# Performance work log

Hardware: AMD Instinct MI355X
Metric: run time of the kernel (lower is better)

Reference implementation:

```python
import jax, jax.numpy as jnp
import numpy as np

EPS = 1e-5
SHARE = 8  # share_planes

def batchnorm(x, gamma, beta):
    # BatchNorm1d over the point (batch) dimension, training-mode stats
    mu = jnp.mean(x, axis=0, keepdims=True)
    var = jnp.var(x, axis=0, keepdims=True)
    return gamma * (x - mu) * jax.lax.rsqrt(var + EPS) + beta

def setup_inputs() -> dict:
    key = jax.random.key(0)
    ks = jax.random.split(key, 12)
    N, K, C = 100000, 16, 64
    s = 0.05
    return {
        "p": jax.random.normal(ks[0], (N, 3), jnp.float32),
        "x": jax.random.normal(ks[1], (N, C), jnp.float32),
        "knn_idx": jax.random.randint(ks[2], (N, K), 0, N, jnp.int32),
        "W1": jax.random.normal(ks[3], (C, C), jnp.float32) * s,
        "Wv": jax.random.normal(ks[4], (C, C), jnp.float32) * s,
        "Wp1": jax.random.normal(ks[5], (3, C), jnp.float32) * s,
        "Wp2": jax.random.normal(ks[6], (C, C), jnp.float32) * s,
        "Ww": jax.random.normal(ks[7], (C, C // SHARE), jnp.float32) * s,
        "W3": jax.random.normal(ks[8], (C, C), jnp.float32) * s,
        "g1": jnp.ones((C,), jnp.float32), "b1": jnp.zeros((C,), jnp.float32),
        "g2": jnp.ones((C,), jnp.float32), "b2": jnp.zeros((C,), jnp.float32),
        "g3": jnp.ones((C,), jnp.float32), "b3": jnp.zeros((C,), jnp.float32),
    }

def reference(p, x, knn_idx, W1, Wv, Wp1, Wp2, Ww, W3, g1, b1, g2, b2, g3, b3):
    # PointMixerBlock: linear1/bn1 -> intra-set mixing/bn2 -> linear3/bn3 + residual
    identity = x
    h = jax.nn.relu(batchnorm(x @ W1, g1, b1))              # [N, C]
    # --- PointMixer intra-set layer (gather-compute-aggregate) ---
    v = h @ Wv                                               # values [N, C]
    pj = p[knn_idx]                                          # [N, K, 3] neighbor coords
    delta = pj - p[:, None, :]                               # relative positions
    e = jax.nn.relu(delta @ Wp1) @ Wp2                       # pos encoding [N, K, C]
    hj = h[knn_idx]                                          # neighbor feats [N, K, C]
    energy = (hj + e) @ Ww                                   # [N, K, C//SHARE]
    w = jax.nn.softmax(energy, axis=1)                       # mix over K neighbors
    w = jnp.repeat(w, SHARE, axis=2)                         # share weights across channel groups
    mixed = jnp.sum(w * (v[knn_idx] + e), axis=1)            # [N, C]
    # -------------------------------------------------------------
    h = jax.nn.relu(batchnorm(mixed, g2, b2))
    h = batchnorm(h @ W3, g3, b3)
    return jax.nn.relu(h + identity)
```

## Files before the change

kernel.cpp:

```cpp
#include <hip/hip_runtime.h>
#include <hip/hip_fp16.h>

#define EPSV 1e-5f
#define PST 2048
#define GRID_GEMM 782
#define GRID_MIX  1024
#define GRID_ELT  1024

typedef _Float16 h2_t  __attribute__((ext_vector_type(2)));
typedef __fp16   fp16x2 __attribute__((ext_vector_type(2)));
typedef _Float16 f16x4 __attribute__((ext_vector_type(4)));
typedef _Float16 f16x8 __attribute__((ext_vector_type(8)));
typedef float    f32x4 __attribute__((ext_vector_type(4)));
typedef unsigned short u16;

__device__ __forceinline__ float frelu(float x) { return fmaxf(x, 0.f); }

__device__ __forceinline__ unsigned int pkrtz(float lo, float hi) {
  fp16x2 h = __builtin_amdgcn_cvt_pkrtz(lo, hi);
  return __builtin_bit_cast(unsigned int, h);
}
__device__ __forceinline__ u16 f16b(float x) {
  return (u16)(pkrtz(x, 0.f) & 0xffffu);
}
__device__ __forceinline__ float f16tof(u16 u) {
  return (float)(*reinterpret_cast<const _Float16*>(&u));
}
__device__ __forceinline__ f16x8 mk8(unsigned a, unsigned b, unsigned c, unsigned d) {
  uint4 u; u.x = a; u.y = b; u.z = c; u.w = d;
  return __builtin_bit_cast(f16x8, u);
}
__device__ __forceinline__ f16x4 mk4(unsigned a, unsigned b) {
  uint2 u; u.x = a; u.y = b;
  return __builtin_bit_cast(f16x4, u);
}
__device__ __forceinline__ f32x4 mfma16(f16x8 a, f16x8 b, f32x4 c) {
  return __builtin_amdgcn_mfma_f32_16x16x32_f16(a, b, c, 0, 0, 0);
}
__device__ __forceinline__ f32x4 mfma16k16(f16x4 a, f16x4 b, f32x4 c) {
  return __builtin_amdgcn_mfma_f32_16x16x16f16(a, b, c, 0, 0, 0);
}
__device__ __forceinline__ unsigned relu2(unsigned u) {
  const unsigned m = ((u & 0x80008000u) >> 15) * 0xFFFFu;
  return u & ~m;
}

__global__ __launch_bounds__(256) void pack_k(
    const float* __restrict__ Wp2, const float* __restrict__ Ww,
    const float* __restrict__ Wp1,
    uint4* __restrict__ wwf, uint4* __restrict__ wp2f, uint4* __restrict__ w1f)
{
  __shared__ float wwl[512];
  const int t = threadIdx.x, a = t >> 2, qq = t & 3;
  float acc[8] = {0,0,0,0,0,0,0,0};
#pragma unroll
  for (int cc = 0; cc < 16; ++cc) {
    const int c = qq*16 + cc;
    const float wv = Wp2[a*64 + c];
#pragma unroll
    for (int g = 0; g < 8; ++g) acc[g] = fmaf(wv, Ww[c*8 + g], acc[g]);
  }
#pragma unroll
  for (int g = 0; g < 8; ++g) {
    acc[g] += __shfl_xor(acc[g], 1);
    acc[g] += __shfl_xor(acc[g], 2);
  }
  if (qq == 0) {
#pragma unroll
    for (int g = 0; g < 8; ++g) wwl[a*8 + g] = acc[g];
  }
  __syncthreads();
  if (t < 128) {
    const int h = t >> 6, l = t & 63, r16 = l & 15, q = l >> 4;
    uint4 u = {0,0,0,0};
    if (r16 < 8) {
      unsigned c0 = pkrtz(wwl[(32*h+8*q+0)*8 + r16], wwl[(32*h+8*q+1)*8 + r16]);
      unsigned c1 = pkrtz(wwl[(32*h+8*q+2)*8 + r16], wwl[(32*h+8*q+3)*8 + r16]);
      unsigned c2 = pkrtz(wwl[(32*h+8*q+4)*8 + r16], wwl[(32*h+8*q+5)*8 + r16]);
      unsigned c3 = pkrtz(wwl[(32*h+8*q+6)*8 + r16], wwl[(32*h+8*q+7)*8 + r16]);
      u.x = c0; u.y = c1; u.z = c2; u.w = c3;
    }
    wwf[t] = u;
  }
  for (int e = t; e < 512; e += 256) {
    const int tt = e >> 7, h = (e >> 6) & 1, l = e & 63;
    const int c = 16*tt + (l & 15), q = l >> 4;
    const int d0 = 32*h + 8*q;
    uint4 u;
    u.x = pkrtz(Wp2[(d0+0)*64 + c], Wp2[(d0+1)*64 + c]);
    u.y = pkrtz(Wp2[(d0+2)*64 + c], Wp2[(d0+3)*64 + c]);
    u.z = pkrtz(Wp2[(d0+4)*64 + c], Wp2[(d0+5)*64 + c]);
    u.w = pkrtz(Wp2[(d0+6)*64 + c], Wp2[(d0+7)*64 + c]);
    wp2f[e] = u;
  }
  for (int e = t; e < 384; e += 256) {
    const int r = e >> 7, h = (e >> 6) & 1, l = e & 63, q = l >> 4;
    const int d0 = 32*h + 8*q;
    uint4 u;
    u.x = pkrtz(Wp1[r*64 + d0+0], Wp1[r*64 + d0+1]);
    u.y = pkrtz(Wp1[r*64 + d0+2], Wp1[r*64 + d0+3]);
    u.z = pkrtz(Wp1[r*64 + d0+4], Wp1[r*64 + d0+5]);
    u.w = pkrtz(Wp1[r*64 + d0+6], Wp1[r*64 + d0+7]);
    w1f[e] = u;
  }
}

template<int MODE, bool INF16>
__global__ __launch_bounds__(256, 4) void gemm_mfma_k(
    const void* __restrict__ in, const float* __restrict__ W,
    const float* __restrict__ Ww, const float* __restrict__ ss,
    u16* __restrict__ out16, u16* __restrict__ outw16,
    float* __restrict__ partials, int N)
{
  __shared__ float red[512];
  __shared__ u16 xh[4][16*72];
  const int t = threadIdx.x, lane = t & 63, w = t >> 6;
  const int r16 = lane & 15, q = lane >> 4;
  u16* const xw = &xh[w][0];

  f16x8 bw[2][4];
#pragma unroll
  for (int kb = 0; kb < 2; ++kb) {
#pragma unroll
    for (int tt = 0; tt < 4; ++tt) {
      const int kbase = 32*kb + 8*q;
      const int cc = 16*tt + r16;
      unsigned u0 = pkrtz(W[(kbase+0)*64 + cc], W[(kbase+1)*64 + cc]);
      unsigned u1 = pkrtz(W[(kbase+2)*64 + cc], W[(kbase+3)*64 + cc]);
      unsigned u2 = pkrtz(W[(kbase+4)*64 + cc], W[(kbase+5)*64 + cc]);
      unsigned u3 = pkrtz(W[(kbase+6)*64 + cc], W[(kbase+7)*64 + cc]);
      bw[kb][tt] = mk8(u0, u1, u2, u3);
    }
  }
  f16x8 bg[2];
  if (MODE == 1) {
#pragma unroll
    for (int kb = 0; kb < 2; ++kb) {
      const int kbase = 32*kb + 8*q;
      unsigned u[4];
#pragma unroll
      for (int mm = 0; mm < 4; ++mm) {
        float g0 = (r16 < 8) ? Ww[(kbase + 2*mm    )*8 + r16] : 0.f;
        float g1 = (r16 < 8) ? Ww[(kbase + 2*mm + 1)*8 + r16] : 0.f;
        u[mm] = pkrtz(g0, g1);
      }
      bg[kb] = mk8(u[0], u[1], u[2], u[3]);
    }
  }
  float sc4[4], sh4[4];
  if (MODE != 0) {
#pragma unroll
    for (int j = 0; j < 4; ++j) {
      sc4[j] = ss[4*r16 + j];
      sh4[j] = ss[64 + 4*r16 + j];
    }
  }

  float S4[4] = {0,0,0,0}, Q4[4] = {0,0,0,0};
  const int ntiles = (N + 15) >> 4;
  for (int tile = blockIdx.x*4 + w; tile < ntiles; tile += GRID_GEMM*4) {
    const int r0 = tile << 4;
    const bool full = (r0 + 16 <= N);
#pragma unroll
    for (int i = 0; i < 4; ++i) {
      const int row = q + 4*i;
      float4 xv = {0.f, 0.f, 0.f, 0.f};
      const bool rok = full || (r0 + row < N);
      if (rok) {
        if constexpr (INF16) {
          const uint2 u = *(const uint2*)((const u16*)in + (size_t)(r0 + row)*64 + 4*r16);
          const h2_t lo = __builtin_bit_cast(h2_t, u.x);
          const h2_t hi = __builtin_bit_cast(h2_t, u.y);
          xv.x = (float)lo[0]; xv.y = (float)lo[1];
          xv.z = (float)hi[0]; xv.w = (float)hi[1];
        } else {
          xv = *(const float4*)((const float*)in + (size_t)(r0 + row)*64 + 4*r16);
        }
      }
      if (MODE != 0) {
        xv.x = frelu(fmaf(xv.x, sc4[0], sh4[0]));
        xv.y = frelu(fmaf(xv.y, sc4[1], sh4[1]));
        xv.z = frelu(fmaf(xv.z, sc4[2], sh4[2]));
        xv.w = frelu(fmaf(xv.w, sc4[3], sh4[3]));
        if (!rok) { xv.x = 0.f; xv.y = 0.f; xv.z = 0.f; xv.w = 0.f; }
      }
      uint2 u2v; u2v.x = pkrtz(xv.x, xv.y); u2v.y = pkrtz(xv.z, xv.w);
      *(uint2*)(xw + row*72 + 4*r16) = u2v;
    }
    const f16x8 a0 = __builtin_bit_cast(f16x8, *(const uint4*)(xw + r16*72 + 8*q));
    const f16x8 a1 = __builtin_bit_cast(f16x8, *(const uint4*)(xw + r16*72 + 8*q + 32));
    f32x4 acc[4];
#pragma unroll
    for (int tt = 0; tt < 4; ++tt) {
      f32x4 z = {0.f, 0.f, 0.f, 0.f};
      z = mfma16(a0, bw[0][tt], z);
      acc[tt] = mfma16(a1, bw[1][tt], z);
    }
#pragma unroll
    for (int tt = 0; tt < 4; ++tt) {
#pragma unroll
      for (int j = 0; j < 4; ++j) {
        if (full || (r0 + 4*q + j < N))
          out16[(size_t)(r0 + 4*q + j)*64 + 16*tt + r16] = f16b(acc[tt][j]);
      }
      if (MODE != 1) {
        S4[tt] += acc[tt][0] + acc[tt][1] + acc[tt][2] + acc[tt][3];
        Q4[tt] = fmaf(acc[tt][0], acc[tt][0], Q4[tt]);
        Q4[tt] = fmaf(acc[tt][1], acc[tt][1], Q4[tt]);
        Q4[tt] = fmaf(acc[tt][2], acc[tt][2], Q4[tt]);
        Q4[tt] = fmaf(acc[tt][3], acc[tt][3], Q4[tt]);
      }
    }
    if (MODE == 1) {
      f32x4 accw = {0.f, 0.f, 0.f, 0.f};
      accw = mfma16(a0, bg[0], accw);
      accw = mfma16(a1, bg[1], accw);
      if (r16 < 8) {
#pragma unroll
        for (int j = 0; j < 4; ++j) {
          if (full || (r0 + 4*q + j < N))
            outw16[(size_t)(r0 + 4*q + j)*8 + r16] = f16b(accw[j]);
        }
      }
    }
  }
  if (MODE != 1) {
#pragma unroll
    for (int tt = 0; tt < 4; ++tt) {
      S4[tt] += __shfl_xor(S4[tt], 16); S4[tt] += __shfl_xor(S4[tt], 32);
      Q4[tt] += __shfl_xor(Q4[tt], 16); Q4[tt] += __shfl_xor(Q4[tt], 32);
    }
    if (lane < 16) {
#pragma unroll
      for (int tt = 0; tt < 4; ++tt) {
        red[w*128 + tt*16 + lane]      = S4[tt];
        red[w*128 + 64 + tt*16 + lane] = Q4[tt];
      }
    }
    __syncthreads();
    if (t < 64) {
      const float s = red[t] + red[128+t] + red[256+t] + red[384+t];
      const float qq = red[64+t] + red[192+t] + red[320+t] + red[448+t];
      partials[(size_t)t*PST + blockIdx.x]      = s;
      partials[(size_t)(64+t)*PST + blockIdx.x] = qq;
    }
  }
}

__global__ __launch_bounds__(256) void fin_k(const float* __restrict__ partials,
    int nblk, const float* __restrict__ gamma, const float* __restrict__ beta,
    float* __restrict__ ss, float invN)
{
  __shared__ float red[8];
  const int c = blockIdx.x;
  float s = 0.f, q = 0.f;
  for (int i = threadIdx.x; i < nblk; i += 256) {
    s += partials[(size_t)c*PST + i];
    q += partials[(size_t)(64+c)*PST + i];
  }
#pragma unroll
  for (int mk = 1; mk < 64; mk <<= 1) {
    s += __shfl_xor(s, mk);
    q += __shfl_xor(q, mk);
  }
  const int w = threadIdx.x >> 6;
  if ((threadIdx.x & 63) == 0) { red[w*2] = s; red[w*2+1] = q; }
  __syncthreads();
  if (threadIdx.x == 0) {
    const float S = red[0]+red[2]+red[4]+red[6];
    const float Q = red[1]+red[3]+red[5]+red[7];
    const float mean = S*invN;
    const float var  = Q*invN - mean*mean;
    const float scale = gamma[c] * rsqrtf(var + EPSV);
    ss[c] = scale; ss[64+c] = beta[c] - mean*scale;
  }
}

__global__ __launch_bounds__(256, 4) void mixer_k(
    const float* __restrict__ p, const int* __restrict__ knn,
    const u16* __restrict__ v16, const u16* __restrict__ hw16,
    const uint4* __restrict__ wwf, const uint4* __restrict__ wp2f,
    const uint4* __restrict__ w1f,
    u16* __restrict__ mx16, float* __restrict__ partials, int N)
{
  __shared__ float red[512];
  const int t = threadIdx.x, lane = t & 63, w = t >> 6;
  const int r16 = lane & 15, q = lane >> 4, b = r16 >> 3;

  f16x8 wwB[2];
  wwB[0] = __builtin_bit_cast(f16x8, wwf[lane]);
  wwB[1] = __builtin_bit_cast(f16x8, wwf[64 + lane]);
  f16x8 wp2B[8];
#pragma unroll
  for (int e = 0; e < 8; ++e)
    wp2B[e] = __builtin_bit_cast(f16x8, wp2f[e*64 + lane]);
  unsigned w1a[6][4];
#pragma unroll
  for (int e = 0; e < 6; ++e) {
    const uint4 u = w1f[e*64 + lane];
    w1a[e][0] = u.x; w1a[e][1] = u.y; w1a[e][2] = u.z; w1a[e][3] = u.w;
  }

  float ssum = 0.f, sq = 0.f;
  const int nwaves = gridDim.x * 4;

  for (int i = blockIdx.x*4 + w; i < N; i += nwaves) {
    const int4 kn4 = *(const int4*)(knn + (size_t)i*16 + 4*q);
    const int kn[4] = {kn4.x, kn4.y, kn4.z, kn4.w};
    const int jj = knn[(size_t)i*16 + r16];
    u16 vt[4][4];
#pragma unroll
    for (int tt = 0; tt < 4; ++tt)
#pragma unroll
      for (int j = 0; j < 4; ++j)
        vt[tt][j] = v16[(size_t)kn[j]*64 + 16*tt + r16];
    u16 hvu[4];
#pragma unroll
    for (int j = 0; j < 4; ++j) hvu[j] = hw16[(size_t)kn[j]*8 + r16];
    const float pix = p[(size_t)i*3], piy = p[(size_t)i*3+1], piz = p[(size_t)i*3+2];
    const float dx = p[(size_t)jj*3]   - pix;
    const float dy = p[(size_t)jj*3+1] - piy;
    const float dz = p[(size_t)jj*3+2] - piz;

    const h2_t dx2 = __builtin_bit_cast(h2_t, pkrtz(dx, dx));
    const h2_t dy2 = __builtin_bit_cast(h2_t, pkrtz(dy, dy));
    const h2_t dz2 = __builtin_bit_cast(h2_t, pkrtz(dz, dz));
    f16x8 eA[2];
#pragma unroll
    for (int h = 0; h < 2; ++h) {
      unsigned eu[4];
#pragma unroll
      for (int mm = 0; mm < 4; ++mm) {
        h2_t acc = dz2 * __builtin_bit_cast(h2_t, w1a[4+h][mm]);
        acc = dy2 * __builtin_bit_cast(h2_t, w1a[2+h][mm]) + acc;
        acc = dx2 * __builtin_bit_cast(h2_t, w1a[0+h][mm]) + acc;
        eu[mm] = relu2(__builtin_bit_cast(unsigned, acc));
      }
      eA[h] = mk8(eu[0], eu[1], eu[2], eu[3]);
    }

    f32x4 en = {0.f, 0.f, 0.f, 0.f};
    en = mfma16(eA[0], wwB[0], en);
    en = mfma16(eA[1], wwB[1], en);
#pragma unroll
    for (int j = 0; j < 4; ++j)
      en[j] += (r16 < 8) ? f16tof(hvu[j]) : 0.f;

    float m = fmaxf(fmaxf(en[0], en[1]), fmaxf(en[2], en[3]));
    m = fmaxf(m, __shfl_xor(m, 16));
    m = fmaxf(m, __shfl_xor(m, 32));
    const float e0 = __expf(en[0]-m), e1 = __expf(en[1]-m);
    const float e2 = __expf(en[2]-m), e3 = __expf(en[3]-m);
    float s = e0 + e1 + e2 + e3;
    s += __shfl_xor(s, 16);
    s += __shfl_xor(s, 32);
    const float rs = 1.f / s;
    const f16x4 aw = mk4(pkrtz(e0*rs, e1*rs), pkrtz(e2*rs, e3*rs));

    float outv = 0.f;
#pragma unroll
    for (int tt = 0; tt < 4; ++tt) {
      f32x4 E = {0.f, 0.f, 0.f, 0.f};
      E = mfma16(eA[0], wp2B[tt*2], E);
      E = mfma16(eA[1], wp2B[tt*2+1], E);
#pragma unroll
      for (int j = 0; j < 4; ++j) E[j] += f16tof(vt[tt][j]);
      const f16x4 bE = mk4(pkrtz(E[0], E[1]), pkrtz(E[2], E[3]));
      f32x4 G = {0.f, 0.f, 0.f, 0.f};
      G = mfma16k16(aw, bE, G);
      const float sel = b ? G[(2*tt+1) & 3] : G[(2*tt) & 3];
      const float val = __shfl(sel, ((tt >= 2) ? 16 : 0) + r16);
      if (q == tt) outv = val;
    }
    mx16[(size_t)i*64 + lane] = f16b(outv);
    ssum += outv; sq = fmaf(outv, outv, sq);
  }
  __syncthreads();
  red[w*128 + lane] = ssum; red[w*128 + 64 + lane] = sq;
  __syncthreads();
  if (t < 64) {
    const float s = red[t] + red[128+t] + red[256+t] + red[384+t];
    const float qv = red[64+t] + red[192+t] + red[320+t] + red[448+t];
    partials[(size_t)t*PST + blockIdx.x]      = s;
    partials[(size_t)(64+t)*PST + blockIdx.x] = qv;
  }
}

__global__ __launch_bounds__(256) void final_k(const u16* __restrict__ y16,
    const float* __restrict__ x, const float* __restrict__ ss,
    float* __restrict__ out, int n4)
{
  __shared__ float sl[128];
  if (threadIdx.x < 128) sl[threadIdx.x] = ss[threadIdx.x];
  __syncthreads();
  for (int idx = blockIdx.x*256 + threadIdx.x; idx < n4; idx += gridDim.x*256) {
    const int cb = (idx & 15) << 2;
    const uint2 yu = *(const uint2*)(y16 + (size_t)idx*4);
    const h2_t ylo = __builtin_bit_cast(h2_t, yu.x);
    const h2_t yhi = __builtin_bit_cast(h2_t, yu.y);
    const float4 xx = ((const float4*)x)[idx];
    float4 o;
    o.x = frelu(fmaf((float)ylo[0], sl[cb],   sl[64+cb])   + xx.x);
    o.y = frelu(fmaf((float)ylo[1], sl[cb+1], sl[64+cb+1]) + xx.y);
    o.z = frelu(fmaf((float)yhi[0], sl[cb+2], sl[64+cb+2]) + xx.z);
    o.w = frelu(fmaf((float)yhi[1], sl[cb+3], sl[64+cb+3]) + xx.w);
    ((float4*)out)[idx] = o;
  }
}

extern "C" void kernel_launch(void* const* d_in, const int* in_sizes, int n_in,
                              void* d_out, int out_size, void* d_ws, size_t ws_size,
                              hipStream_t stream)
{
  (void)n_in; (void)out_size; (void)ws_size;
  const float* p   = (const float*)d_in[0];
  const float* x   = (const float*)d_in[1];
  const int*   knn = (const int*)  d_in[2];
  const float* W1  = (const float*)d_in[3];
  const float* Wv  = (const float*)d_in[4];
  const float* Wp1 = (const float*)d_in[5];
  const float* Wp2 = (const float*)d_in[6];
  const float* Ww  = (const float*)d_in[7];
  const float* W3  = (const float*)d_in[8];
  const float* g1  = (const float*)d_in[9];
  const float* b1  = (const float*)d_in[10];
  const float* g2  = (const float*)d_in[11];
  const float* b2  = (const float*)d_in[12];
  const float* g3  = (const float*)d_in[13];
  const float* b3  = (const float*)d_in[14];
  const int N = in_sizes[0] / 3;
  const float invN = 1.f / (float)N;

  u16* ws16 = (u16*)d_ws;
  u16* y16   = ws16;
  u16* v16   = y16 + (size_t)N*64;
  u16* mx16  = v16 + (size_t)N*64;
  u16* hw16  = mx16 + (size_t)N*64;
  uint4* fr  = (uint4*)(hw16 + (size_t)N*8);
  uint4* wwf  = fr;
  uint4* wp2f = fr + 128;
  uint4* w1f  = fr + 640;
  float* partials = (float*)(fr + 1024);
  float* ss1      = partials + (size_t)128*PST;
  float* ss2      = ss1 + 128;
  float* ss3      = ss2 + 128;

  pack_k<<<1, 256, 0, stream>>>(Wp2, Ww, Wp1, wwf, wp2f, w1f);
  gemm_mfma_k<0, false><<<GRID_GEMM, 256, 0, stream>>>(x, W1, nullptr, nullptr, y16, nullptr, partials, N);
  fin_k<<<64, 256, 0, stream>>>(partials, GRID_GEMM, g1, b1, ss1, invN);
  gemm_mfma_k<1, true><<<GRID_GEMM, 256, 0, stream>>>(y16, Wv, Ww, ss1, v16, hw16, nullptr, N);
  mixer_k<<<GRID_MIX, 256, 0, stream>>>(p, knn, v16, hw16, wwf, wp2f, w1f, mx16, partials, N);
  fin_k<<<64, 256, 0, stream>>>(partials, GRID_MIX, g2, b2, ss2, invN);
  gemm_mfma_k<2, true><<<GRID_GEMM, 256, 0, stream>>>(mx16, W3, nullptr, ss2, y16, nullptr, partials, N);
  fin_k<<<64, 256, 0, stream>>>(partials, GRID_GEMM, g3, b3, ss3, invN);
  final_k<<<GRID_ELT, 256, 0, stream>>>(y16, x, ss3, (float*)d_out, N*16);
}
```

Baseline: 119.7 us.

## Fold weight packing into first GEMM launch, double grid sizes, reorder gather loop

Removes the separate single-block pack_k launch by running the weight-packing work in an extra block of the first GEMM kernel. Doubles the grid sizes of the GEMM, mixer and elementwise kernels to raise parallelism and occupancy. Reorders the mixer's neighbor-value gather loop so each neighbor row's loads are issued together. More blocks means more partial-sum rows for the BN reductions (PST is 2048, so GRID_MIX=2048 fits exactly), and the packing block could extend the first kernel's tail.

Result: slower. 122.2 us (+2.0%).

```diff
diff --git a/kernel.cpp b/kernel.cpp
--- a/kernel.cpp
+++ b/kernel.cpp
@@ -3,9 +3,9 @@
 
 #define EPSV 1e-5f
 #define PST 2048
-#define GRID_GEMM 782
-#define GRID_MIX  1024
-#define GRID_ELT  1024
+#define GRID_GEMM 1563
+#define GRID_MIX  2048
+#define GRID_ELT  2048
 
 typedef _Float16 h2_t  __attribute__((ext_vector_type(2)));
 typedef __fp16   fp16x2 __attribute__((ext_vector_type(2)));
@@ -45,79 +45,79 @@
   return u & ~m;
 }
 
-__global__ __launch_bounds__(256) void pack_k(
-    const float* __restrict__ Wp2, const float* __restrict__ Ww,
-    const float* __restrict__ Wp1,
-    uint4* __restrict__ wwf, uint4* __restrict__ wp2f, uint4* __restrict__ w1f)
-{
-  __shared__ float wwl[512];
-  const int t = threadIdx.x, a = t >> 2, qq = t & 3;
-  float acc[8] = {0,0,0,0,0,0,0,0};
-#pragma unroll
-  for (int cc = 0; cc < 16; ++cc) {
-    const int c = qq*16 + cc;
-    const float wv = Wp2[a*64 + c];
-#pragma unroll
-    for (int g = 0; g < 8; ++g) acc[g] = fmaf(wv, Ww[c*8 + g], acc[g]);
-  }
-#pragma unroll
-  for (int g = 0; g < 8; ++g) {
-    acc[g] += __shfl_xor(acc[g], 1);
-    acc[g] += __shfl_xor(acc[g], 2);
-  }
-  if (qq == 0) {
-#pragma unroll
-    for (int g = 0; g < 8; ++g) wwl[a*8 + g] = acc[g];
-  }
-  __syncthreads();
-  if (t < 128) {
-    const int h = t >> 6, l = t & 63, r16 = l & 15, q = l >> 4;
-    uint4 u = {0,0,0,0};
-    if (r16 < 8) {
-      unsigned c0 = pkrtz(wwl[(32*h+8*q+0)*8 + r16], wwl[(32*h+8*q+1)*8 + r16]);
-      unsigned c1 = pkrtz(wwl[(32*h+8*q+2)*8 + r16], wwl[(32*h+8*q+3)*8 + r16]);
-      unsigned c2 = pkrtz(wwl[(32*h+8*q+4)*8 + r16], wwl[(32*h+8*q+5)*8 + r16]);
-      unsigned c3 = pkrtz(wwl[(32*h+8*q+6)*8 + r16], wwl[(32*h+8*q+7)*8 + r16]);
-      u.x = c0; u.y = c1; u.z = c2; u.w = c3;
-    }
-    wwf[t] = u;
-  }
-  for (int e = t; e < 512; e += 256) {
-    const int tt = e >> 7, h = (e >> 6) & 1, l = e & 63;
-    const int c = 16*tt + (l & 15), q = l >> 4;
-    const int d0 = 32*h + 8*q;
-    uint4 u;
-    u.x = pkrtz(Wp2[(d0+0)*64 + c], Wp2[(d0+1)*64 + c]);
-    u.y = pkrtz(Wp2[(d0+2)*64 + c], Wp2[(d0+3)*64 + c]);
-    u.z = pkrtz(Wp2[(d0+4)*64 + c], Wp2[(d0+5)*64 + c]);
-    u.w = pkrtz(Wp2[(d0+6)*64 + c], Wp2[(d0+7)*64 + c]);
-    wp2f[e] = u;
-  }
-  for (int e = t; e < 384; e += 256) {
-    const int r = e >> 7, h = (e >> 6) & 1, l = e & 63, q = l >> 4;
-    const int d0 = 32*h + 8*q;
-    uint4 u;
-    u.x = pkrtz(Wp1[r*64 + d0+0], Wp1[r*64 + d0+1]);
-    u.y = pkrtz(Wp1[r*64 + d0+2], Wp1[r*64 + d0+3]);
-    u.z = pkrtz(Wp1[r*64 + d0+4], Wp1[r*64 + d0+5]);
-    u.w = pkrtz(Wp1[r*64 + d0+6], Wp1[r*64 + d0+7]);
-    w1f[e] = u;
-  }
-}
-
 template<int MODE, bool INF16>
 __global__ __launch_bounds__(256, 4) void gemm_mfma_k(
     const void* __restrict__ in, const float* __restrict__ W,
     const float* __restrict__ Ww, const float* __restrict__ ss,
     u16* __restrict__ out16, u16* __restrict__ outw16,
-    float* __restrict__ partials, int N)
+    float* __restrict__ partials, int N,
+    const float* __restrict__ Wp2, const float* __restrict__ Wp1,
+    uint4* __restrict__ wwf, uint4* __restrict__ wp2f, uint4* __restrict__ w1f)
 {
   __shared__ float red[512];
   __shared__ u16 xh[4][16*72];
   const int t = threadIdx.x, lane = t & 63, w = t >> 6;
   const int r16 = lane & 15, q = lane >> 4;
+
+  if (MODE == 0 && blockIdx.x == GRID_GEMM) {
+    float* wwl = (float*)&xh[0][0];
+    {
+      const int a = t >> 2, qq = t & 3;
+      float acc[8] = {0,0,0,0,0,0,0,0};
+#pragma unroll
+      for (int cc = 0; cc < 16; ++cc) {
+        const int c = qq*16 + cc;
+        const float wv = Wp2[a*64 + c];
+#pragma unroll
+        for (int g = 0; g < 8; ++g) acc[g] = fmaf(wv, Ww[c*8 + g], acc[g]);
+      }
+#pragma unroll
+      for (int g = 0; g < 8; ++g) {
+        acc[g] += __shfl_xor(acc[g], 1);
+        acc[g] += __shfl_xor(acc[g], 2);
+      }
+      if (qq == 0) {
+#pragma unroll
+        for (int g = 0; g < 8; ++g) wwl[a*8 + g] = acc[g];
+      }
+    }
+    __syncthreads();
+    if (t < 128) {
+      const int h = t >> 6, l = t & 63, rr = l & 15, qq = l >> 4;
+      uint4 u = {0,0,0,0};
+      if (rr < 8) {
+        u.x = pkrtz(wwl[(32*h+8*qq+0)*8 + rr], wwl[(32*h+8*qq+1)*8 + rr]);
+        u.y = pkrtz(wwl[(32*h+8*qq+2)*8 + rr], wwl[(32*h+8*qq+3)*8 + rr]);
+        u.z = pkrtz(wwl[(32*h+8*qq+4)*8 + rr], wwl[(32*h+8*qq+5)*8 + rr]);
+        u.w = pkrtz(wwl[(32*h+8*qq+6)*8 + rr], wwl[(32*h+8*qq+7)*8 + rr]);
+      }
+      wwf[t] = u;
+    }
+    for (int e = t; e < 512; e += 256) {
+      const int tt = e >> 7, h = (e >> 6) & 1, l = e & 63;
+      const int c = 16*tt + (l & 15), qq = l >> 4;
+      const int d0 = 32*h + 8*qq;
+      uint4 u;
+      u.x = pkrtz(Wp2[(d0+0)*64 + c], Wp2[(d0+1)*64 + c]);
+      u.y = pkrtz(Wp2[(d0+2)*64 + c], Wp2[(d0+3)*64 + c]);
+      u.z = pkrtz(Wp2[(d0+4)*64 + c], Wp2[(d0+5)*64 + c]);
+      u.w = pkrtz(Wp2[(d0+6)*64 + c], Wp2[(d0+7)*64 + c]);
+      wp2f[e] = u;
+    }
+    for (int e = t; e < 384; e += 256) {
+      const int r = e >> 7, h = (e >> 6) & 1, l = e & 63, qq = l >> 4;
+      const int d0 = 32*h + 8*qq;
+      uint4 u;
+      u.x = pkrtz(Wp1[r*64 + d0+0], Wp1[r*64 + d0+1]);
+      u.y = pkrtz(Wp1[r*64 + d0+2], Wp1[r*64 + d0+3]);
+      u.z = pkrtz(Wp1[r*64 + d0+4], Wp1[r*64 + d0+5]);
+      u.w = pkrtz(Wp1[r*64 + d0+6], Wp1[r*64 + d0+7]);
+      w1f[e] = u;
+    }
+    return;
+  }
+
   u16* const xw = &xh[w][0];
-
   f16x8 bw[2][4];
 #pragma unroll
   for (int kb = 0; kb < 2; ++kb) {
@@ -310,10 +310,11 @@
     const int jj = knn[(size_t)i*16 + r16];
     u16 vt[4][4];
 #pragma unroll
-    for (int tt = 0; tt < 4; ++tt)
-#pragma unroll
-      for (int j = 0; j < 4; ++j)
-        vt[tt][j] = v16[(size_t)kn[j]*64 + 16*tt + r16];
+    for (int j = 0; j < 4; ++j) {
+      const u16* vp = v16 + (size_t)kn[j]*64 + r16;
+#pragma unroll
+      for (int tt = 0; tt < 4; ++tt) vt[tt][j] = vp[16*tt];
+    }
     u16 hvu[4];
 #pragma unroll
     for (int j = 0; j < 4; ++j) hvu[j] = hw16[(size_t)kn[j]*8 + r16];
@@ -445,13 +446,15 @@
   float* ss2      = ss1 + 128;
   float* ss3      = ss2 + 128;
 
-  pack_k<<<1, 256, 0, stream>>>(Wp2, Ww, Wp1, wwf, wp2f, w1f);
-  gemm_mfma_k<0, false><<<GRID_GEMM, 256, 0, stream>>>(x, W1, nullptr, nullptr, y16, nullptr, partials, N);
+  gemm_mfma_k<0, false><<<GRID_GEMM + 1, 256, 0, stream>>>(
+      x, W1, Ww, nullptr, y16, nullptr, partials, N, Wp2, Wp1, wwf, wp2f, w1f);
   fin_k<<<64, 256, 0, stream>>>(partials, GRID_GEMM, g1, b1, ss1, invN);
-  gemm_mfma_k<1, true><<<GRID_GEMM, 256, 0, stream>>>(y16, Wv, Ww, ss1, v16, hw16, nullptr, N);
+  gemm_mfma_k<1, true><<<GRID_GEMM, 256, 0, stream>>>(
+      y16, Wv, Ww, ss1, v16, hw16, nullptr, N, nullptr, nullptr, nullptr, nullptr, nullptr);
   mixer_k<<<GRID_MIX, 256, 0, stream>>>(p, knn, v16, hw16, wwf, wp2f, w1f, mx16, partials, N);
   fin_k<<<64, 256, 0, stream>>>(partials, GRID_MIX, g2, b2, ss2, invN);
-  gemm_mfma_k<2, true><<<GRID_GEMM, 256, 0, stream>>>(mx16, W3, nullptr, ss2, y16, nullptr, partials, N);
+  gemm_mfma_k<2, true><<<GRID_GEMM, 256, 0, stream>>>(
+      mx16, W3, nullptr, ss2, y16, nullptr, partials, N, nullptr, nullptr, nullptr, nullptr, nullptr);
   fin_k<<<64, 256, 0, stream>>>(partials, GRID_GEMM, g3, b3, ss3, invN);
   final_k<<<GRID_ELT, 256, 0, stream>>>(y16, x, ss3, (float*)d_out, N*16);
 }
```
